# Kernel tuning notes

Measured on AMD Instinct MI355X. Metric: run time of the kernel, lower is better.

Reference implementation:

```python
import math
import jax, jax.numpy as jnp
import numpy as np

B, T, C = 8, 1024, 768
H = 12
D = C // H  # 64


def setup_inputs() -> dict:
    key = jax.random.key(0)
    k1, k2, k3, k4, k5 = jax.random.split(key, 5)
    s = 0.02
    return {
        "x": jax.random.normal(k1, (B, T, C), dtype=jnp.float32),
        "w_qkv": jax.random.normal(k2, (C, 3 * C), dtype=jnp.float32) * s,
        "b_qkv": jax.random.normal(k3, (3 * C,), dtype=jnp.float32) * s,
        "w_proj": jax.random.normal(k4, (C, C), dtype=jnp.float32) * s,
        "b_proj": jax.random.normal(k5, (C,), dtype=jnp.float32) * s,
    }


def reference(x, w_qkv, b_qkv, w_proj, b_proj):
    b, t, c = x.shape
    qkv = x @ w_qkv + b_qkv                      # [B,T,3C]
    q, k, v = jnp.split(qkv, 3, axis=-1)
    # [B,T,C] -> [B,H,T,D]
    q = q.reshape(b, t, H, D).transpose(0, 2, 1, 3)
    k = k.reshape(b, t, H, D).transpose(0, 2, 1, 3)
    v = v.reshape(b, t, H, D).transpose(0, 2, 1, 3)
    scale = 1.0 / math.sqrt(D)
    att = jnp.einsum("bhqd,bhkd->bhqk", q, k) * scale   # [B,H,T,T]
    causal = jnp.tril(jnp.ones((t, t), dtype=bool))
    att = jnp.where(causal, att, -jnp.inf)
    att = jax.nn.softmax(att, axis=-1)
    y = jnp.einsum("bhqk,bhkd->bhqd", att, v)            # [B,H,T,D]
    y = y.transpose(0, 2, 1, 3).reshape(b, t, c)
    return y @ w_proj + b_proj
```

## Files before the change

### kernel.cpp

```cpp
#include <hip/hip_runtime.h>
#include <math.h>

#define B_ 8
#define T_ 1024
#define C_ 768
#define H_ 12
#define D_ 64

typedef __bf16 bf16x8 __attribute__((ext_vector_type(8)));
typedef float  f32x4  __attribute__((ext_vector_type(4)));
typedef unsigned short us8 __attribute__((ext_vector_type(8)));
typedef unsigned int   u32x4v __attribute__((ext_vector_type(4)));

typedef __attribute__((address_space(3))) void lds_void;
typedef __attribute__((address_space(1))) const void glb_void;

#define KSC 0.18033688011112043f

__device__ __forceinline__ unsigned short f2bf(float f) {
    unsigned int u = __float_as_uint(f);
    u += 0x7fffu + ((u >> 16) & 1u);
    return (unsigned short)(u >> 16);
}

__global__ __launch_bounds__(256)
void convert_bf16(const float* __restrict__ in, unsigned short* __restrict__ out, int n4) {
    int idx = blockIdx.x * 256 + threadIdx.x;
    if (idx < n4) {
        float4 v = ((const float4*)in)[idx];
        ushort4 o;
        o.x = f2bf(v.x); o.y = f2bf(v.y); o.z = f2bf(v.z); o.w = f2bf(v.w);
        ((ushort4*)out)[idx] = o;
    }
}

__global__ __launch_bounds__(256)
void scale_bias(const float* __restrict__ in, float* __restrict__ out) {
    int i = blockIdx.x * 256 + threadIdx.x;
    if (i < 3 * C_) out[i] = in[i] * (i < C_ ? KSC : 1.f);
}

__global__ __launch_bounds__(256)
void transpose_w(const float* __restrict__ W, unsigned short* __restrict__ Wt,
                 int K, int N, int nlim, float qs) {
    __shared__ unsigned short Ts[64][65];
    const int n0 = blockIdx.x * 64, k0 = blockIdx.y * 64;
    for (int i = threadIdx.x; i < 4096; i += 256) {
        int n = i & 63, k = i >> 6;
        float sc = (n0 + n < nlim) ? qs : 1.f;
        Ts[n][k] = f2bf(W[(size_t)(k0 + k) * N + n0 + n] * sc);
    }
    __syncthreads();
    for (int i = threadIdx.x; i < 4096; i += 256) {
        int k = i & 63, n = i >> 6;
        Wt[(size_t)(n0 + n) * K + k0 + k] = Ts[n][k];
    }
}

template<int OUT_BF16>
__global__ __launch_bounds__(256)
void gemm_bf16_bt(const unsigned short* __restrict__ A,
                  const unsigned short* __restrict__ Bt,
                  const float* __restrict__ bias,
                  void* __restrict__ Cout,
                  int M, int N, int K) {
    __shared__ __align__(16) unsigned short As[4096];
    __shared__ __align__(16) unsigned short Bs[4096];

    const int tid  = threadIdx.x;
    const int lane = tid & 63;
    const int c    = lane & 15;
    const int quad = lane >> 4;
    const int wave = tid >> 6;
    const int wm   = (wave >> 1) * 64;
    const int wn   = (wave & 1) * 64;
    const int bm   = blockIdx.y * 128;
    const int bn   = blockIdx.x * 128;

    const int Lp0 = tid;
    const int Lp1 = 256 + tid;
    const int L0  = Lp0 ^ ((Lp0 >> 3) & 7);
    const int L1  = Lp1 ^ ((Lp1 >> 3) & 7);
    const unsigned short* aSrc0 = A  + (size_t)(bm + (L0 >> 2)) * K + (L0 & 3) * 8;
    const unsigned short* aSrc1 = A  + (size_t)(bm + (L1 >> 2)) * K + (L1 & 3) * 8;
    const unsigned short* bSrc0 = Bt + (size_t)(bn + (L0 >> 2)) * K + (L0 & 3) * 8;
    const unsigned short* bSrc1 = Bt + (size_t)(bn + (L1 >> 2)) * K + (L1 & 3) * 8;
    unsigned short* ldsA0 = As + (tid & 0xC0) * 8;
    unsigned short* ldsA1 = As + (256 + (tid & 0xC0)) * 8;
    unsigned short* ldsB0 = Bs + (tid & 0xC0) * 8;
    unsigned short* ldsB1 = Bs + (256 + (tid & 0xC0)) * 8;

    const int xorv = (c >> 1) & 7;
    int aoff[4], boff[4];
#pragma unroll
    for (int i = 0; i < 4; i++) {
        aoff[i] = ((((wm + i * 16 + c) << 2) + quad) ^ xorv) * 8;
        boff[i] = ((((wn + i * 16 + c) << 2) + quad) ^ xorv) * 8;
    }

    f32x4 acc[4][4];
#pragma unroll
    for (int i = 0; i < 4; i++)
#pragma unroll
        for (int j = 0; j < 4; j++) acc[i][j] = (f32x4){0.f, 0.f, 0.f, 0.f};

    for (int kt = 0; kt < K; kt += 32) {
        __syncthreads();
        __builtin_amdgcn_global_load_lds((glb_void*)aSrc0, (lds_void*)ldsA0, 16, 0, 0);
        __builtin_amdgcn_global_load_lds((glb_void*)aSrc1, (lds_void*)ldsA1, 16, 0, 0);
        __builtin_amdgcn_global_load_lds((glb_void*)bSrc0, (lds_void*)ldsB0, 16, 0, 0);
        __builtin_amdgcn_global_load_lds((glb_void*)bSrc1, (lds_void*)ldsB1, 16, 0, 0);
        aSrc0 += 32; aSrc1 += 32; bSrc0 += 32; bSrc1 += 32;
        __syncthreads();

        bf16x8 af[4], bfr[4];
#pragma unroll
        for (int i = 0; i < 4; i++)
            af[i] = __builtin_bit_cast(bf16x8, *(const us8*)&As[aoff[i]]);
#pragma unroll
        for (int j = 0; j < 4; j++)
            bfr[j] = __builtin_bit_cast(bf16x8, *(const us8*)&Bs[boff[j]]);
#pragma unroll
        for (int i = 0; i < 4; i++)
#pragma unroll
            for (int j = 0; j < 4; j++)
                acc[i][j] = __builtin_amdgcn_mfma_f32_16x16x32_bf16(af[i], bfr[j], acc[i][j], 0, 0, 0);
    }

    float bs[4];
#pragma unroll
    for (int j = 0; j < 4; j++) bs[j] = bias[bn + wn + j * 16 + c];
#pragma unroll
    for (int i = 0; i < 4; i++) {
        const int gm = bm + wm + i * 16 + quad * 4;
#pragma unroll
        for (int r = 0; r < 4; r++) {
            const size_t ro = (size_t)(gm + r) * N;
#pragma unroll
            for (int j = 0; j < 4; j++) {
                const float v = acc[i][j][r] + bs[j];
                const int gn = bn + wn + j * 16 + c;
                if (OUT_BF16) ((unsigned short*)Cout)[ro + gn] = f2bf(v);
                else          ((float*)Cout)[ro + gn] = v;
            }
        }
    }
}

__device__ __forceinline__ int sigmaK(int k) {
    return 16 * (2 * (k >> 5) + ((k >> 2) & 1)) + 4 * ((k >> 3) & 3) + (k & 3);
}

__global__ __launch_bounds__(256, 3)
void attn_mfma(const unsigned short* __restrict__ qkv, unsigned short* __restrict__ y) {
    __shared__ __align__(16) unsigned short Ks[64 * 72];
    __shared__ __align__(16) unsigned int   Vt[64 * 36];

    const int tid  = threadIdx.x;
    const int wave = tid >> 6;
    const int lane = tid & 63;
    const int c    = lane & 15;
    const int quad = lane >> 4;

    const int id = blockIdx.x;
    const int p  = (id >> 3) & 7;
    const int bh = (id >> 6) * 8 + (id & 7);
    const int b  = bh / H_;
    const int h  = bh - b * H_;

    const int qts[2] = {p, 15 - p};
    const int q0s[2] = {p * 64, (15 - p) * 64};

    const int RS = 3 * C_;
    const unsigned short* kbase = qkv + (size_t)b * T_ * RS + C_ + h * D_;
    const unsigned short* vbase = qkv + (size_t)b * T_ * RS + 2 * C_ + h * D_;

    bf16x8 qf[2][2];
#pragma unroll
    for (int t = 0; t < 2; t++) {
        const unsigned short* qrow =
            qkv + ((size_t)(b * T_ + q0s[t] + wave * 16 + c)) * RS + h * D_ + quad * 8;
        qf[t][0] = __builtin_bit_cast(bf16x8, *(const us8*)qrow);
        qf[t][1] = __builtin_bit_cast(bf16x8, *(const us8*)(qrow + 32));
    }

    const int kr0 = tid >> 3, kc0 = tid & 7;
    const int sK0 = sigmaK(kr0) * 72 + kc0 * 8;
    const int sK1 = sigmaK(kr0 + 32) * 72 + kc0 * 8;
    const int dg  = tid >> 4, kp0 = tid & 15;

    us8 kA, kB;
    ushort4 vA0, vB0, vA1, vB1;
    {
        kA = *(const us8*)(kbase + (size_t)kr0 * RS + kc0 * 8);
        kB = *(const us8*)(kbase + (size_t)(kr0 + 32) * RS + kc0 * 8);
        const unsigned short* p0 = vbase + (size_t)(2 * kp0) * RS + dg * 4;
        vA0 = *(const ushort4*)p0;  vB0 = *(const ushort4*)(p0 + RS);
        const unsigned short* p1 = vbase + (size_t)(2 * (kp0 + 16)) * RS + dg * 4;
        vA1 = *(const ushort4*)p1;  vB1 = *(const ushort4*)(p1 + RS);
    }

    f32x4 Oa[2][4];
    float l_lane[2] = {0.f, 0.f};
#pragma unroll
    for (int t = 0; t < 2; t++)
#pragma unroll
        for (int d = 0; d < 4; d++) Oa[t][d] = (f32x4){0.f, 0.f, 0.f, 0.f};

    const int ktEnd = qts[1];
    for (int kt = 0; kt <= ktEnd; kt++) {
        __syncthreads();
        *(us8*)&Ks[sK0] = kA;
        *(us8*)&Ks[sK1] = kB;
        {
            unsigned int* v0 = &Vt[(dg * 4) * 36 + kp0];
            v0[0]   = vA0.x | ((unsigned)vB0.x << 16);
            v0[36]  = vA0.y | ((unsigned)vB0.y << 16);
            v0[72]  = vA0.z | ((unsigned)vB0.z << 16);
            v0[108] = vA0.w | ((unsigned)vB0.w << 16);
            unsigned int* v1 = v0 + 16;
            v1[0]   = vA1.x | ((unsigned)vB1.x << 16);
            v1[36]  = vA1.y | ((unsigned)vB1.y << 16);
            v1[72]  = vA1.z | ((unsigned)vB1.z << 16);
            v1[108] = vA1.w | ((unsigned)vB1.w << 16);
        }
        __syncthreads();

        if (kt < ktEnd) {
            const unsigned short* kp = kbase + (size_t)((kt + 1) * 64) * RS;
            kA = *(const us8*)(kp + (size_t)kr0 * RS + kc0 * 8);
            kB = *(const us8*)(kp + (size_t)(kr0 + 32) * RS + kc0 * 8);
            const unsigned short* vp = vbase + (size_t)((kt + 1) * 64) * RS;
            const unsigned short* p0 = vp + (size_t)(2 * kp0) * RS + dg * 4;
            vA0 = *(const ushort4*)p0;  vB0 = *(const ushort4*)(p0 + RS);
            const unsigned short* p1 = vp + (size_t)(2 * (kp0 + 16)) * RS + dg * 4;
            vA1 = *(const ushort4*)p1;  vB1 = *(const ushort4*)(p1 + RS);
        }

        bf16x8 kf[4][2];
#pragma unroll
        for (int nb = 0; nb < 4; nb++) {
#pragma unroll
            for (int ks = 0; ks < 2; ks++)
                kf[nb][ks] = __builtin_bit_cast(bf16x8,
                    *(const us8*)&Ks[(nb * 16 + c) * 72 + quad * 8 + ks * 32]);
        }

#pragma unroll
        for (int t = 0; t < 2; t++) {
            if (kt > qts[t]) continue;
            const bool diag = (kt == qts[t]);
            const int nbmax = diag ? ((wave >= 2) ? 3 : 1) : 3;

            f32x4 sv[4];
#pragma unroll
            for (int nb = 0; nb < 4; nb++) {
                if (nb <= nbmax) {
                    f32x4 z = (f32x4){0.f, 0.f, 0.f, 0.f};
                    z = __builtin_amdgcn_mfma_f32_16x16x32_bf16(kf[nb][0], qf[t][0], z, 0, 0, 0);
                    sv[nb] = __builtin_amdgcn_mfma_f32_16x16x32_bf16(kf[nb][1], qf[t][1], z, 0, 0, 0);
                }
            }
            if (diag) {
                const int qloc = wave * 16 + c;
#pragma unroll
                for (int nb = 0; nb < 4; nb++) {
                    if (nb <= nbmax) {
                        const int kb = 32 * (nb >> 1) + 4 * (nb & 1) + 8 * quad;
#pragma unroll
                        for (int r = 0; r < 4; r++)
                            if (kb + r > qloc) sv[nb][r] = -INFINITY;
                    }
                }
            }

            float rsum = 0.f;
            unsigned int pd[4][2];
#pragma unroll
            for (int nb = 0; nb < 4; nb++) {
                if (nb <= nbmax) {
                    float p0 = __builtin_amdgcn_exp2f(sv[nb][0]);
                    float p1 = __builtin_amdgcn_exp2f(sv[nb][1]);
                    float p2 = __builtin_amdgcn_exp2f(sv[nb][2]);
                    float p3 = __builtin_amdgcn_exp2f(sv[nb][3]);
                    rsum += (p0 + p1) + (p2 + p3);
                    unsigned u0 = __float_as_uint(p0) + 0x8000u;
                    unsigned u1 = __float_as_uint(p1) + 0x8000u;
                    unsigned u2 = __float_as_uint(p2) + 0x8000u;
                    unsigned u3 = __float_as_uint(p3) + 0x8000u;
                    pd[nb][0] = (u0 >> 16) | (u1 & 0xffff0000u);
                    pd[nb][1] = (u2 >> 16) | (u3 & 0xffff0000u);
                } else {
                    pd[nb][0] = 0u; pd[nb][1] = 0u;
                }
            }
            l_lane[t] += rsum;

            bf16x8 ap0 = __builtin_bit_cast(bf16x8,
                (u32x4v){pd[0][0], pd[0][1], pd[1][0], pd[1][1]});
            bf16x8 ap1 = __builtin_bit_cast(bf16x8,
                (u32x4v){pd[2][0], pd[2][1], pd[3][0], pd[3][1]});
#pragma unroll
            for (int dd = 0; dd < 4; dd++) {
                const unsigned int* vrow = &Vt[(dd * 16 + c) * 36 + quad * 4];
                bf16x8 vb0 = __builtin_bit_cast(bf16x8, *(const u32x4v*)vrow);
                bf16x8 vb1 = __builtin_bit_cast(bf16x8, *(const u32x4v*)(vrow + 16));
                Oa[t][dd] = __builtin_amdgcn_mfma_f32_16x16x32_bf16(ap0, vb0, Oa[t][dd], 0, 0, 0);
                Oa[t][dd] = __builtin_amdgcn_mfma_f32_16x16x32_bf16(ap1, vb1, Oa[t][dd], 0, 0, 0);
            }
        }
    }

#pragma unroll
    for (int t = 0; t < 2; t++) {
        float lr = l_lane[t];
        lr += __shfl_xor(lr, 16, 64);
        lr += __shfl_xor(lr, 32, 64);
        unsigned short* yrow =
            y + ((size_t)(b * T_ + q0s[t] + wave * 16)) * C_ + h * D_;
#pragma unroll
        for (int r = 0; r < 4; r++) {
            float lq  = __shfl(lr, quad * 4 + r, 64);
            float inv = 1.f / lq;
#pragma unroll
            for (int dd = 0; dd < 4; dd++)
                yrow[(size_t)(quad * 4 + r) * C_ + dd * 16 + c] = f2bf(Oa[t][dd][r] * inv);
        }
    }
}

extern "C" void kernel_launch(void* const* d_in, const int* in_sizes, int n_in,
                              void* d_out, int out_size, void* d_ws, size_t ws_size,
                              hipStream_t stream) {
    const float* x      = (const float*)d_in[0];
    const float* w_qkv  = (const float*)d_in[1];
    const float* b_qkv  = (const float*)d_in[2];
    const float* w_proj = (const float*)d_in[3];
    const float* b_proj = (const float*)d_in[4];
    float* out = (float*)d_out;

    unsigned short* xb   = (unsigned short*)d_ws;
    unsigned short* wqT  = xb   + (size_t)B_ * T_ * C_;
    unsigned short* wpT  = wqT  + (size_t)3 * C_ * C_;
    unsigned short* qkvb = wpT  + (size_t)C_ * C_;
    unsigned short* yb   = qkvb + (size_t)B_ * T_ * 3 * C_;
    float*          bqs  = (float*)(yb + (size_t)B_ * T_ * C_);

    const int nx4 = B_ * T_ * C_ / 4;
    convert_bf16<<<(nx4 + 255) / 256, 256, 0, stream>>>(x, xb, nx4);
    scale_bias<<<(3 * C_ + 255) / 256, 256, 0, stream>>>(b_qkv, bqs);
    transpose_w<<<dim3(3 * C_ / 64, C_ / 64), 256, 0, stream>>>(w_qkv, wqT, C_, 3 * C_, C_, KSC);
    transpose_w<<<dim3(C_ / 64, C_ / 64), 256, 0, stream>>>(w_proj, wpT, C_, C_, 0, 1.f);

    gemm_bf16_bt<1><<<dim3(3 * C_ / 128, B_ * T_ / 128), 256, 0, stream>>>(
        xb, wqT, bqs, qkvb, B_ * T_, 3 * C_, C_);

    attn_mfma<<<8 * B_ * H_, 256, 0, stream>>>(qkvb, yb);

    gemm_bf16_bt<0><<<dim3(C_ / 128, B_ * T_ / 128), 256, 0, stream>>>(
        yb, wpT, b_proj, out, B_ * T_, C_, C_);
}
```

Measured before the change: 201.7 us.

## Fuse prep kernels, deepen GEMM K-tile, compute softmax denominators via MFMA

Merges the four preprocessing kernels into one launch that dispatches on block index. In the GEMM, each K step grows from 32 to 64, halving the number of barrier pairs, and the grid is reordered so blockIdx.x walks M. In attention, the row-sum of probabilities is computed with an MFMA against a ones vector instead of scalar adds and shuffles, and the upper half of the PV MFMAs is skipped on diagonal tiles where those probabilities are zero. LDS use per GEMM block doubles, which may lower occupancy.

After: 189.7 us. 5.9% less time.

```diff
diff --git a/kernel.cpp b/kernel.cpp
--- a/kernel.cpp
+++ b/kernel.cpp
@@ -24,36 +24,43 @@
 }
 
 __global__ __launch_bounds__(256)
-void convert_bf16(const float* __restrict__ in, unsigned short* __restrict__ out, int n4) {
-    int idx = blockIdx.x * 256 + threadIdx.x;
-    if (idx < n4) {
-        float4 v = ((const float4*)in)[idx];
+void prep_all(const float* __restrict__ x, const float* __restrict__ w_qkv,
+              const float* __restrict__ b_qkv, const float* __restrict__ w_proj,
+              unsigned short* __restrict__ xb, unsigned short* __restrict__ wqT,
+              unsigned short* __restrict__ wpT, float* __restrict__ bqs) {
+    __shared__ unsigned short Ts[64][65];
+    const int id  = blockIdx.x;
+    const int tid = threadIdx.x;
+    if (id < 6144) {
+        int idx = id * 256 + tid;
+        float4 v = ((const float4*)x)[idx];
         ushort4 o;
         o.x = f2bf(v.x); o.y = f2bf(v.y); o.z = f2bf(v.z); o.w = f2bf(v.w);
-        ((ushort4*)out)[idx] = o;
-    }
-}
-
-__global__ __launch_bounds__(256)
-void scale_bias(const float* __restrict__ in, float* __restrict__ out) {
-    int i = blockIdx.x * 256 + threadIdx.x;
-    if (i < 3 * C_) out[i] = in[i] * (i < C_ ? KSC : 1.f);
-}
-
-__global__ __launch_bounds__(256)
-void transpose_w(const float* __restrict__ W, unsigned short* __restrict__ Wt,
-                 int K, int N, int nlim, float qs) {
-    __shared__ unsigned short Ts[64][65];
-    const int n0 = blockIdx.x * 64, k0 = blockIdx.y * 64;
-    for (int i = threadIdx.x; i < 4096; i += 256) {
-        int n = i & 63, k = i >> 6;
-        float sc = (n0 + n < nlim) ? qs : 1.f;
-        Ts[n][k] = f2bf(W[(size_t)(k0 + k) * N + n0 + n] * sc);
-    }
-    __syncthreads();
-    for (int i = threadIdx.x; i < 4096; i += 256) {
-        int k = i & 63, n = i >> 6;
-        Wt[(size_t)(n0 + n) * K + k0 + k] = Ts[n][k];
+        ((ushort4*)xb)[idx] = o;
+        return;
+    }
+    if (id < 6729) {
+        const float* W; unsigned short* Wt; int N, nlim, t2;
+        if (id < 6576) { t2 = id - 6144; W = w_qkv;  Wt = wqT; N = 3 * C_; nlim = C_;
+            ;
+        } else if (id < 6720) { t2 = id - 6576; W = w_proj; Wt = wpT; N = C_; nlim = 0;
+        } else {
+            int i = (id - 6720) * 256 + tid;
+            if (i < 3 * C_) bqs[i] = b_qkv[i] * (i < C_ ? KSC : 1.f);
+            return;
+        }
+        const int ntiles = N / 64;
+        const int n0 = (t2 % ntiles) * 64, k0 = (t2 / ntiles) * 64;
+        for (int i = tid; i < 4096; i += 256) {
+            int n = i & 63, k = i >> 6;
+            float sc = (n0 + n < nlim) ? KSC : 1.f;
+            Ts[n][k] = f2bf(W[(size_t)(k0 + k) * N + n0 + n] * sc);
+        }
+        __syncthreads();
+        for (int i = tid; i < 4096; i += 256) {
+            int k = i & 63, n = i >> 6;
+            Wt[(size_t)(n0 + n) * 768 + k0 + k] = Ts[n][k];
+        }
     }
 }
 
@@ -64,8 +71,8 @@
                   const float* __restrict__ bias,
                   void* __restrict__ Cout,
                   int M, int N, int K) {
-    __shared__ __align__(16) unsigned short As[4096];
-    __shared__ __align__(16) unsigned short Bs[4096];
+    __shared__ __align__(16) unsigned short As[8192];
+    __shared__ __align__(16) unsigned short Bs[8192];
 
     const int tid  = threadIdx.x;
     const int lane = tid & 63;
@@ -74,29 +81,29 @@
     const int wave = tid >> 6;
     const int wm   = (wave >> 1) * 64;
     const int wn   = (wave & 1) * 64;
-    const int bm   = blockIdx.y * 128;
-    const int bn   = blockIdx.x * 128;
-
-    const int Lp0 = tid;
-    const int Lp1 = 256 + tid;
-    const int L0  = Lp0 ^ ((Lp0 >> 3) & 7);
-    const int L1  = Lp1 ^ ((Lp1 >> 3) & 7);
-    const unsigned short* aSrc0 = A  + (size_t)(bm + (L0 >> 2)) * K + (L0 & 3) * 8;
-    const unsigned short* aSrc1 = A  + (size_t)(bm + (L1 >> 2)) * K + (L1 & 3) * 8;
-    const unsigned short* bSrc0 = Bt + (size_t)(bn + (L0 >> 2)) * K + (L0 & 3) * 8;
-    const unsigned short* bSrc1 = Bt + (size_t)(bn + (L1 >> 2)) * K + (L1 & 3) * 8;
-    unsigned short* ldsA0 = As + (tid & 0xC0) * 8;
-    unsigned short* ldsA1 = As + (256 + (tid & 0xC0)) * 8;
-    unsigned short* ldsB0 = Bs + (tid & 0xC0) * 8;
-    unsigned short* ldsB1 = Bs + (256 + (tid & 0xC0)) * 8;
-
-    const int xorv = (c >> 1) & 7;
-    int aoff[4], boff[4];
-#pragma unroll
-    for (int i = 0; i < 4; i++) {
-        aoff[i] = ((((wm + i * 16 + c) << 2) + quad) ^ xorv) * 8;
-        boff[i] = ((((wn + i * 16 + c) << 2) + quad) ^ xorv) * 8;
-    }
+    const int bm   = blockIdx.x * 128;
+    const int bn   = blockIdx.y * 128;
+
+    const unsigned short* aS[4];
+    const unsigned short* bS[4];
+#pragma unroll
+    for (int p = 0; p < 4; p++) {
+        int Lp = p * 256 + tid;
+        int L  = Lp ^ ((Lp >> 3) & 7);
+        aS[p] = A  + (size_t)(bm + (L >> 3)) * K + (L & 7) * 8;
+        bS[p] = Bt + (size_t)(bn + (L >> 3)) * K + (L & 7) * 8;
+    }
+    const int wb = (tid & 0xC0) * 8;
+
+    int aoff[4][2], boff[4][2];
+#pragma unroll
+    for (int i = 0; i < 4; i++)
+#pragma unroll
+        for (int ks = 0; ks < 2; ks++) {
+            const int kcA = (ks * 4 + quad) ^ (c & 7);
+            aoff[i][ks] = ((wm + i * 16 + c) * 8 + kcA) * 8;
+            boff[i][ks] = ((wn + i * 16 + c) * 8 + kcA) * 8;
+        }
 
     f32x4 acc[4][4];
 #pragma unroll
@@ -104,27 +111,32 @@
 #pragma unroll
         for (int j = 0; j < 4; j++) acc[i][j] = (f32x4){0.f, 0.f, 0.f, 0.f};
 
-    for (int kt = 0; kt < K; kt += 32) {
-        __syncthreads();
-        __builtin_amdgcn_global_load_lds((glb_void*)aSrc0, (lds_void*)ldsA0, 16, 0, 0);
-        __builtin_amdgcn_global_load_lds((glb_void*)aSrc1, (lds_void*)ldsA1, 16, 0, 0);
-        __builtin_amdgcn_global_load_lds((glb_void*)bSrc0, (lds_void*)ldsB0, 16, 0, 0);
-        __builtin_amdgcn_global_load_lds((glb_void*)bSrc1, (lds_void*)ldsB1, 16, 0, 0);
-        aSrc0 += 32; aSrc1 += 32; bSrc0 += 32; bSrc1 += 32;
-        __syncthreads();
-
-        bf16x8 af[4], bfr[4];
-#pragma unroll
-        for (int i = 0; i < 4; i++)
-            af[i] = __builtin_bit_cast(bf16x8, *(const us8*)&As[aoff[i]]);
-#pragma unroll
-        for (int j = 0; j < 4; j++)
-            bfr[j] = __builtin_bit_cast(bf16x8, *(const us8*)&Bs[boff[j]]);
-#pragma unroll
-        for (int i = 0; i < 4; i++)
+    for (int kt = 0; kt < K; kt += 64) {
+        __syncthreads();
+#pragma unroll
+        for (int p = 0; p < 4; p++) {
+            __builtin_amdgcn_global_load_lds((glb_void*)aS[p],
+                (lds_void*)(As + p * 2048 + wb), 16, 0, 0);
+            __builtin_amdgcn_global_load_lds((glb_void*)bS[p],
+                (lds_void*)(Bs + p * 2048 + wb), 16, 0, 0);
+            aS[p] += 64; bS[p] += 64;
+        }
+        __syncthreads();
+#pragma unroll
+        for (int ks = 0; ks < 2; ks++) {
+            bf16x8 af[4], bfr[4];
+#pragma unroll
+            for (int i = 0; i < 4; i++)
+                af[i] = __builtin_bit_cast(bf16x8, *(const us8*)&As[aoff[i][ks]]);
 #pragma unroll
             for (int j = 0; j < 4; j++)
-                acc[i][j] = __builtin_amdgcn_mfma_f32_16x16x32_bf16(af[i], bfr[j], acc[i][j], 0, 0, 0);
+                bfr[j] = __builtin_bit_cast(bf16x8, *(const us8*)&Bs[boff[j][ks]]);
+#pragma unroll
+            for (int i = 0; i < 4; i++)
+#pragma unroll
+                for (int j = 0; j < 4; j++)
+                    acc[i][j] = __builtin_amdgcn_mfma_f32_16x16x32_bf16(af[i], bfr[j], acc[i][j], 0, 0, 0);
+        }
     }
 
     float bs[4];
@@ -174,6 +186,9 @@
     const int RS = 3 * C_;
     const unsigned short* kbase = qkv + (size_t)b * T_ * RS + C_ + h * D_;
     const unsigned short* vbase = qkv + (size_t)b * T_ * RS + 2 * C_ + h * D_;
+
+    const u32x4v onesu = {0x3F803F80u, 0x3F803F80u, 0x3F803F80u, 0x3F803F80u};
+    const bf16x8 onesf = __builtin_bit_cast(bf16x8, onesu);
 
     bf16x8 qf[2][2];
 #pragma unroll
@@ -201,11 +216,13 @@
     }
 
     f32x4 Oa[2][4];
-    float l_lane[2] = {0.f, 0.f};
-#pragma unroll
-    for (int t = 0; t < 2; t++)
+    f32x4 Ol[2];
+#pragma unroll
+    for (int t = 0; t < 2; t++) {
+        Ol[t] = (f32x4){0.f, 0.f, 0.f, 0.f};
 #pragma unroll
         for (int d = 0; d < 4; d++) Oa[t][d] = (f32x4){0.f, 0.f, 0.f, 0.f};
+    }
 
     const int ktEnd = qts[1];
     for (int kt = 0; kt <= ktEnd; kt++) {
@@ -250,6 +267,7 @@
         for (int t = 0; t < 2; t++) {
             if (kt > qts[t]) continue;
             const bool diag = (kt == qts[t]);
+            const bool doHi = !diag || (wave >= 2);
             const int nbmax = diag ? ((wave >= 2) ? 3 : 1) : 3;
 
             f32x4 sv[4];
@@ -274,7 +292,6 @@
                 }
             }
 
-            float rsum = 0.f;
             unsigned int pd[4][2];
 #pragma unroll
             for (int nb = 0; nb < 4; nb++) {
@@ -283,7 +300,6 @@
                     float p1 = __builtin_amdgcn_exp2f(sv[nb][1]);
                     float p2 = __builtin_amdgcn_exp2f(sv[nb][2]);
                     float p3 = __builtin_amdgcn_exp2f(sv[nb][3]);
-                    rsum += (p0 + p1) + (p2 + p3);
                     unsigned u0 = __float_as_uint(p0) + 0x8000u;
                     unsigned u1 = __float_as_uint(p1) + 0x8000u;
                     unsigned u2 = __float_as_uint(p2) + 0x8000u;
@@ -294,34 +310,36 @@
                     pd[nb][0] = 0u; pd[nb][1] = 0u;
                 }
             }
-            l_lane[t] += rsum;
 
             bf16x8 ap0 = __builtin_bit_cast(bf16x8,
                 (u32x4v){pd[0][0], pd[0][1], pd[1][0], pd[1][1]});
             bf16x8 ap1 = __builtin_bit_cast(bf16x8,
                 (u32x4v){pd[2][0], pd[2][1], pd[3][0], pd[3][1]});
+
+            Ol[t] = __builtin_amdgcn_mfma_f32_16x16x32_bf16(ap0, onesf, Ol[t], 0, 0, 0);
+            if (doHi)
+                Ol[t] = __builtin_amdgcn_mfma_f32_16x16x32_bf16(ap1, onesf, Ol[t], 0, 0, 0);
+
 #pragma unroll
             for (int dd = 0; dd < 4; dd++) {
                 const unsigned int* vrow = &Vt[(dd * 16 + c) * 36 + quad * 4];
                 bf16x8 vb0 = __builtin_bit_cast(bf16x8, *(const u32x4v*)vrow);
-                bf16x8 vb1 = __builtin_bit_cast(bf16x8, *(const u32x4v*)(vrow + 16));
                 Oa[t][dd] = __builtin_amdgcn_mfma_f32_16x16x32_bf16(ap0, vb0, Oa[t][dd], 0, 0, 0);
-                Oa[t][dd] = __builtin_amdgcn_mfma_f32_16x16x32_bf16(ap1, vb1, Oa[t][dd], 0, 0, 0);
+                if (doHi) {
+                    bf16x8 vb1 = __builtin_bit_cast(bf16x8, *(const u32x4v*)(vrow + 16));
+                    Oa[t][dd] = __builtin_amdgcn_mfma_f32_16x16x32_bf16(ap1, vb1, Oa[t][dd], 0, 0, 0);
+                }
             }
         }
     }
 
 #pragma unroll
     for (int t = 0; t < 2; t++) {
-        float lr = l_lane[t];
-        lr += __shfl_xor(lr, 16, 64);
-        lr += __shfl_xor(lr, 32, 64);
         unsigned short* yrow =
             y + ((size_t)(b * T_ + q0s[t] + wave * 16)) * C_ + h * D_;
 #pragma unroll
         for (int r = 0; r < 4; r++) {
-            float lq  = __shfl(lr, quad * 4 + r, 64);
-            float inv = 1.f / lq;
+            float inv = 1.f / Ol[t][r];
 #pragma unroll
             for (int dd = 0; dd < 4; dd++)
                 yrow[(size_t)(quad * 4 + r) * C_ + dd * 16 + c] = f2bf(Oa[t][dd][r] * inv);
@@ -346,17 +364,13 @@
     unsigned short* yb   = qkvb + (size_t)B_ * T_ * 3 * C_;
     float*          bqs  = (float*)(yb + (size_t)B_ * T_ * C_);
 
-    const int nx4 = B_ * T_ * C_ / 4;
-    convert_bf16<<<(nx4 + 255) / 256, 256, 0, stream>>>(x, xb, nx4);
-    scale_bias<<<(3 * C_ + 255) / 256, 256, 0, stream>>>(b_qkv, bqs);
-    transpose_w<<<dim3(3 * C_ / 64, C_ / 64), 256, 0, stream>>>(w_qkv, wqT, C_, 3 * C_, C_, KSC);
-    transpose_w<<<dim3(C_ / 64, C_ / 64), 256, 0, stream>>>(w_proj, wpT, C_, C_, 0, 1.f);
-
-    gemm_bf16_bt<1><<<dim3(3 * C_ / 128, B_ * T_ / 128), 256, 0, stream>>>(
+    prep_all<<<6729, 256, 0, stream>>>(x, w_qkv, b_qkv, w_proj, xb, wqT, wpT, bqs);
+
+    gemm_bf16_bt<1><<<dim3(B_ * T_ / 128, 3 * C_ / 128), 256, 0, stream>>>(
         xb, wqT, bqs, qkvb, B_ * T_, 3 * C_, C_);
 
     attn_mfma<<<8 * B_ * H_, 256, 0, stream>>>(qkvb, yb);
 
-    gemm_bf16_bt<0><<<dim3(C_ / 128, B_ * T_ / 128), 256, 0, stream>>>(
+    gemm_bf16_bt<0><<<dim3(B_ * T_ / 128, C_ / 128), 256, 0, stream>>>(
         yb, wpT, b_proj, out, B_ * T_, C_, C_);
 }
```
